# Kernel optimization log

Measured on AMD Instinct MI355X. Metric: run time of the kernel, lower is better.

## Reference

```python
import jax, jax.numpy as jnp
import numpy as np

TAU = 1.0
EPS = 1e-8


def setup_inputs() -> dict:
    key = jax.random.key(0)
    ks = jax.random.split(key, 9)
    B, S, D, R, T = 32, 512, 768, 16, 10
    return {
        "x": jax.random.normal(ks[0], (B, S, D), jnp.float32),
        "A_q": jax.random.normal(ks[1], (T, R, D), jnp.float32),
        "B_q": jax.random.normal(ks[2], (T, D, R), jnp.float32),
        "A_v": jax.random.normal(ks[3], (T, R, D), jnp.float32),
        "B_v": jax.random.normal(ks[4], (T, D, R), jnp.float32),
        "qkv_w": jax.random.normal(ks[5], (3 * D, D), jnp.float32) * 0.02,
        "qkv_b": jax.random.normal(ks[6], (3 * D,), jnp.float32) * 0.02,
        "gate_logits": jax.random.normal(ks[7], (T,), jnp.float32),
        "alpha": jax.random.normal(ks[8], (T,), jnp.float32),
    }


def _delta(x, A, B, coef):
    # A: [T,r,d] (torch Linear weight), B: [T,d,r]
    # per-adapter normalized output: (x @ A_t^T @ B_t^T) / (||A_t||_F * ||B_t||_F + eps)
    norm = (jnp.sqrt(jnp.sum(A * A, axis=(1, 2)))
            * jnp.sqrt(jnp.sum(B * B, axis=(1, 2))) + EPS)  # [T]
    w = coef / norm  # [T], folds beta_t * alpha_t / norm_t into the contraction
    h = jnp.einsum('bsd,trd->bstr', x, A)          # [B,S,T,r] tiny rank intermediate
    return jnp.einsum('bstr,t,tdr->bsd', h, w, B)  # weighted sum over tasks


def reference(x, A_q, B_q, A_v, B_v, qkv_w, qkv_b, gate_logits, alpha):
    # deterministic gate: beta = softmax(logits / tau) (Gumbel noise omitted for a
    # reproducible reference of delta = sum_t beta_t * alpha_t * normalized_adapter_t)
    beta = jax.nn.softmax(gate_logits / TAU)
    coef = beta * alpha
    delta_q = _delta(x, A_q, B_q, coef)
    delta_v = _delta(x, A_v, B_v, coef)
    qkv = jnp.einsum('bsd,ed->bse', x, qkv_w) + qkv_b  # [B,S,3D]
    D = x.shape[-1]
    qkv = qkv.at[..., :D].add(delta_q)
    qkv = qkv.at[..., -D:].add(delta_v)
    return qkv
```

## Files before the change

### kernel.cpp

```cpp
#include <hip/hip_runtime.h>

typedef unsigned short u16;
typedef unsigned int   u32;
typedef __bf16 bf16x8 __attribute__((ext_vector_type(8)));
typedef float  f32x4  __attribute__((ext_vector_type(4)));

#define N_TOT 2304

__device__ __forceinline__ u16 f32_to_bf16(float f) {
  u32 u = __float_as_uint(f);
  u32 r = (u + 0x7FFFu + ((u >> 16) & 1u)) >> 16;
  return (u16)r;
}
__device__ __forceinline__ float bf16_to_f32(u16 h) {
  return __uint_as_float(((u32)h) << 16);
}

__device__ __forceinline__ void gload_lds16(const void* gsrc, void* lds) {
  __builtin_amdgcn_global_load_lds(
      (const __attribute__((address_space(1))) void*)gsrc,
      (__attribute__((address_space(3))) void*)lds, 16, 0, 0);
}

__global__ void norms_kernel(const float* __restrict__ Aq, const float* __restrict__ Bq,
                             const float* __restrict__ Av, const float* __restrict__ Bv,
                             float* __restrict__ sumsq) {
  int b = blockIdx.x;
  int which = b / 10, t = b % 10;
  const float* src =
      (which == 0 ? Aq : which == 1 ? Bq : which == 2 ? Av : Bv) + t * 12288;
  float s = 0.f;
  for (int i = threadIdx.x; i < 12288; i += 256) { float v = src[i]; s += v * v; }
  for (int off = 32; off > 0; off >>= 1) s += __shfl_down(s, off, 64);
  __shared__ float red[4];
  if ((threadIdx.x & 63) == 0) red[threadIdx.x >> 6] = s;
  __syncthreads();
  if (threadIdx.x == 0) sumsq[b] = red[0] + red[1] + red[2] + red[3];
}

__global__ void weights_kernel(const float* __restrict__ logits, const float* __restrict__ alpha,
                               const float* __restrict__ sumsq,
                               float* __restrict__ wq, float* __restrict__ wv) {
  int t = threadIdx.x;
  if (t >= 10) return;
  float m = -1e30f;
  for (int i = 0; i < 10; ++i) m = fmaxf(m, logits[i]);
  float sum = 0.f;
  for (int i = 0; i < 10; ++i) sum += expf(logits[i] - m);
  float coef = (expf(logits[t] - m) / sum) * alpha[t];
  wq[t] = coef / (sqrtf(sumsq[t])      * sqrtf(sumsq[10 + t]) + 1e-8f);
  wv[t] = coef / (sqrtf(sumsq[20 + t]) * sqrtf(sumsq[30 + t]) + 1e-8f);
}

__global__ __launch_bounds__(256) void build_weff(
    const float* __restrict__ qkv_w,
    const float* __restrict__ Aq, const float* __restrict__ Bq,
    const float* __restrict__ Av, const float* __restrict__ Bv,
    const float* __restrict__ wq, const float* __restrict__ wv,
    u16* __restrict__ Whi, u16* __restrict__ Wlo) {
  __shared__ float As[160][64];
  __shared__ float Bs[160][32];
  __shared__ float wsh[16];

  const int k0 = blockIdx.x * 64;
  const int n0 = blockIdx.y * 32;
  const int tid = threadIdx.x;
  const int nl = tid >> 3;
  const int kg = tid & 7;

  float acc[8] = {0, 0, 0, 0, 0, 0, 0, 0};
  const bool is_q = (n0 < 768);
  const bool is_v = (n0 >= 1536);
  if (is_q || is_v) {
    const float* A  = is_q ? Aq : Av;
    const float* Bm = is_q ? Bq : Bv;
    const float* w  = is_q ? wq : wv;
    const int noff = is_q ? n0 : (n0 - 1536);
    for (int i = tid; i < 10240; i += 256)
      As[i >> 6][i & 63] = A[(i >> 6) * 768 + k0 + (i & 63)];
    for (int i = tid; i < 5120; i += 256) {
      int tr = i >> 5, n = i & 31;
      Bs[tr][n] = Bm[(tr >> 4) * 12288 + (noff + n) * 16 + (tr & 15)];
    }
    if (tid < 10) wsh[tid] = w[tid];
    __syncthreads();
    for (int tr = 0; tr < 160; ++tr) {
      float wb = wsh[tr >> 4] * Bs[tr][nl];
#pragma unroll
      for (int j = 0; j < 8; ++j) acc[j] += wb * As[tr][kg * 8 + j];
    }
  }
  const int n = n0 + nl;
  const size_t base = (size_t)n * 768 + k0 + kg * 8;
#pragma unroll
  for (int j = 0; j < 8; ++j) {
    float v = qkv_w[base + j] + acc[j];
    u16 h = f32_to_bf16(v);
    u16 l = f32_to_bf16(v - bf16_to_f32(h));
    Whi[base + j] = h;
    Wlo[base + j] = l;
  }
}

__global__ void split_x(const float* __restrict__ x, u16* __restrict__ Xhi, u16* __restrict__ Xlo) {
  int i4 = blockIdx.x * 256 + threadIdx.x;
  if (i4 >= 3145728) return;
  float4 v = ((const float4*)x)[i4];
  u32 h0 = f32_to_bf16(v.x), h1 = f32_to_bf16(v.y), h2 = f32_to_bf16(v.z), h3 = f32_to_bf16(v.w);
  u32 l0 = f32_to_bf16(v.x - bf16_to_f32((u16)h0));
  u32 l1 = f32_to_bf16(v.y - bf16_to_f32((u16)h1));
  u32 l2 = f32_to_bf16(v.z - bf16_to_f32((u16)h2));
  u32 l3 = f32_to_bf16(v.w - bf16_to_f32((u16)h3));
  ((uint2*)Xhi)[i4] = make_uint2(h0 | (h1 << 16), h2 | (h3 << 16));
  ((uint2*)Xlo)[i4] = make_uint2(l0 | (l1 << 16), l2 | (l3 << 16));
}

__global__ __launch_bounds__(512, 2) void gemm_kc(
    const u16* __restrict__ Xhi, const u16* __restrict__ Xlo,
    const u16* __restrict__ Whi, const u16* __restrict__ Wlo,
    const float* __restrict__ bias, float* __restrict__ out) {
  extern __shared__ char smem[];

  const int tid  = threadIdx.x;
  const int lane = tid & 63;
  const int wid  = tid >> 6;

  const int bid = blockIdx.x;
  const int swz = (bid & 7) * 72 + (bid >> 3);
  const int m0 = (swz / 9) << 8;
  const int n0 = (swz % 9) << 8;

  const int wm = (wid >> 2) << 7;
  const int wn = (wid & 3) << 6;
  const int fl = lane & 15, fs = lane >> 4;

  int aFrag[8], bFrag[4];
#pragma unroll
  for (int i = 0; i < 8; ++i) {
    int R = wm + i * 16 + fl;
    int pr = R >> 1;
    int u = (fs + ((R & 1) << 2)) ^ (pr & 7);
    aFrag[i] = (pr * 8 + u) * 16;
  }
#pragma unroll
  for (int j = 0; j < 4; ++j) {
    int R = wn + j * 16 + fl;
    int pr = R >> 1;
    int u = (fs + ((R & 1) << 2)) ^ (pr & 7);
    bFrag[j] = (pr * 8 + u) * 16;
  }

  int ldsByte[2];
  long aSrcOff[2], bSrcOff[2];
#pragma unroll
  for (int jj = 0; jj < 2; ++jj) {
    int P = jj * 512 + tid;
    int pr = P >> 3, p = P & 7;
    int u = p ^ (pr & 7);
    int r = (pr << 1) | (u >> 2);
    int s = u & 3;
    ldsByte[jj]  = P * 16;
    aSrcOff[jj] = (long)(m0 + r) * 768 + s * 8;
    bSrcOff[jj] = (long)(n0 + r) * 768 + s * 8;
  }

  auto stage = [&](int t2, int bufi) {
    int tc = t2 > 71 ? 71 : t2;
    int reg = tc / 24;
    int ksrc = (tc - reg * 24) << 5;
    const u16* xb = (reg == 2) ? Xlo : Xhi;
    const u16* wb = (reg == 1) ? Wlo : Whi;
    char* base = smem + bufi * 32768;
    gload_lds16(xb + aSrcOff[0] + ksrc, base + ldsByte[0]);
    gload_lds16(xb + aSrcOff[1] + ksrc, base + ldsByte[1]);
    gload_lds16(wb + bSrcOff[0] + ksrc, base + 16384 + ldsByte[0]);
    gload_lds16(wb + bSrcOff[1] + ksrc, base + 16384 + ldsByte[1]);
  };

  f32x4 acc[8][4] = {};

  stage(0, 0);
  stage(1, 1);
  asm volatile("s_waitcnt vmcnt(4)" ::: "memory");
  __builtin_amdgcn_sched_barrier(0);
  __builtin_amdgcn_s_barrier();

  for (int t = 0; t < 72; ++t) {
    char* bufA = smem + (t & 3) * 32768;
    char* bufB = bufA + 16384;
    bf16x8 a[8], b[4];
#pragma unroll
    for (int i = 0; i < 8; ++i) a[i] = *(const bf16x8*)(bufA + aFrag[i]);
#pragma unroll
    for (int j = 0; j < 4; ++j) b[j] = *(const bf16x8*)(bufB + bFrag[j]);

    stage(t + 2, (t + 2) & 3);
    asm volatile("s_waitcnt vmcnt(4)" ::: "memory");
    __builtin_amdgcn_sched_barrier(0);
    __builtin_amdgcn_s_barrier();

    __builtin_amdgcn_s_setprio(1);
#pragma unroll
    for (int i = 0; i < 8; ++i)
#pragma unroll
      for (int j = 0; j < 4; ++j)
        acc[i][j] = __builtin_amdgcn_mfma_f32_16x16x32_bf16(a[i], b[j], acc[i][j], 0, 0, 0);
    __builtin_amdgcn_s_setprio(0);
  }

#pragma unroll
  for (int j = 0; j < 4; ++j) {
    const int n = n0 + wn + j * 16 + fl;
    const float bj = bias[n];
#pragma unroll
    for (int i = 0; i < 8; ++i) {
      const int mbase = m0 + wm + i * 16 + (fs << 2);
#pragma unroll
      for (int r = 0; r < 4; ++r)
        out[(size_t)(mbase + r) * N_TOT + n] = acc[i][j][r] + bj;
    }
  }
}

extern "C" void kernel_launch(void* const* d_in, const int* in_sizes, int n_in,
                              void* d_out, int out_size, void* d_ws, size_t ws_size,
                              hipStream_t stream) {
  const float* x     = (const float*)d_in[0];
  const float* Aq    = (const float*)d_in[1];
  const float* Bq    = (const float*)d_in[2];
  const float* Av    = (const float*)d_in[3];
  const float* Bv    = (const float*)d_in[4];
  const float* qkvw  = (const float*)d_in[5];
  const float* qkvb  = (const float*)d_in[6];
  const float* gate  = (const float*)d_in[7];
  const float* alpha = (const float*)d_in[8];
  float* out = (float*)d_out;

  char* ws = (char*)d_ws;
  float* sumsq = (float*)ws;
  float* wq    = (float*)(ws + 256);
  float* wv    = (float*)(ws + 512);
  u16* Whi = (u16*)(ws + 1024);
  u16* Wlo = Whi + 1769472;
  u16* Xhi = Wlo + 1769472;
  u16* Xlo = Xhi + 12582912;

  static bool attr_set = false;
  if (!attr_set) {
    hipFuncSetAttribute((const void*)gemm_kc,
                        hipFuncAttributeMaxDynamicSharedMemorySize, 131072);
    attr_set = true;
  }

  hipLaunchKernelGGL(norms_kernel,   dim3(40),     dim3(256), 0, stream, Aq, Bq, Av, Bv, sumsq);
  hipLaunchKernelGGL(weights_kernel, dim3(1),      dim3(64),  0, stream, gate, alpha, sumsq, wq, wv);
  hipLaunchKernelGGL(build_weff,     dim3(12, 72), dim3(256), 0, stream, qkvw, Aq, Bq, Av, Bv, wq, wv, Whi, Wlo);
  hipLaunchKernelGGL(split_x,        dim3(12288),  dim3(256), 0, stream, x, Xhi, Xlo);
  hipLaunchKernelGGL(gemm_kc,        dim3(576),    dim3(512), 131072, stream,
                     Xhi, Xlo, Whi, Wlo, qkvb, out);
}
```

Before: 447.4 us.

## Split GEMM main loop into two barrier-fenced phases interleaving LDS reads with MFMA

Splits each K-step of the GEMM main loop into two halves. The first half loads four A fragments and all B fragments, issues the next stage's global-to-LDS loads, then runs 16 MFMAs. The second half loads the remaining four A fragments and runs the other 16 MFMAs. Extra workgroup barriers and explicit lgkmcnt waits enforce a ping-pong style schedule across waves, so LDS reads of one wave can overlap MFMAs of another and peak register pressure drops. The cost is two additional s_barriers per iteration. The attribute-caching flag in the host launcher is also removed, so hipFuncSetAttribute is called on every launch.

```diff
diff --git a/kernel.cpp b/kernel.cpp
--- a/kernel.cpp
+++ b/kernel.cpp
@@ -184,28 +184,77 @@
   asm volatile("s_waitcnt vmcnt(4)" ::: "memory");
   __builtin_amdgcn_sched_barrier(0);
   __builtin_amdgcn_s_barrier();
+  __builtin_amdgcn_sched_barrier(0);
 
   for (int t = 0; t < 72; ++t) {
     char* bufA = smem + (t & 3) * 32768;
     char* bufB = bufA + 16384;
-    bf16x8 a[8], b[4];
-#pragma unroll
-    for (int i = 0; i < 8; ++i) a[i] = *(const bf16x8*)(bufA + aFrag[i]);
-#pragma unroll
-    for (int j = 0; j < 4; ++j) b[j] = *(const bf16x8*)(bufB + bFrag[j]);
-
+
+    bf16x8 a0 = *(const bf16x8*)(bufA + aFrag[0]);
+    bf16x8 a1 = *(const bf16x8*)(bufA + aFrag[1]);
+    bf16x8 a2 = *(const bf16x8*)(bufA + aFrag[2]);
+    bf16x8 a3 = *(const bf16x8*)(bufA + aFrag[3]);
+    bf16x8 b0 = *(const bf16x8*)(bufB + bFrag[0]);
+    bf16x8 b1 = *(const bf16x8*)(bufB + bFrag[1]);
+    bf16x8 b2 = *(const bf16x8*)(bufB + bFrag[2]);
+    bf16x8 b3 = *(const bf16x8*)(bufB + bFrag[3]);
     stage(t + 2, (t + 2) & 3);
+    __builtin_amdgcn_sched_barrier(0);
+    __builtin_amdgcn_s_barrier();
+    asm volatile("s_waitcnt lgkmcnt(0)" ::: "memory");
+    __builtin_amdgcn_sched_barrier(0);
+    __builtin_amdgcn_s_setprio(1);
+    acc[0][0] = __builtin_amdgcn_mfma_f32_16x16x32_bf16(a0, b0, acc[0][0], 0, 0, 0);
+    acc[0][1] = __builtin_amdgcn_mfma_f32_16x16x32_bf16(a0, b1, acc[0][1], 0, 0, 0);
+    acc[0][2] = __builtin_amdgcn_mfma_f32_16x16x32_bf16(a0, b2, acc[0][2], 0, 0, 0);
+    acc[0][3] = __builtin_amdgcn_mfma_f32_16x16x32_bf16(a0, b3, acc[0][3], 0, 0, 0);
+    acc[1][0] = __builtin_amdgcn_mfma_f32_16x16x32_bf16(a1, b0, acc[1][0], 0, 0, 0);
+    acc[1][1] = __builtin_amdgcn_mfma_f32_16x16x32_bf16(a1, b1, acc[1][1], 0, 0, 0);
+    acc[1][2] = __builtin_amdgcn_mfma_f32_16x16x32_bf16(a1, b2, acc[1][2], 0, 0, 0);
+    acc[1][3] = __builtin_amdgcn_mfma_f32_16x16x32_bf16(a1, b3, acc[1][3], 0, 0, 0);
+    acc[2][0] = __builtin_amdgcn_mfma_f32_16x16x32_bf16(a2, b0, acc[2][0], 0, 0, 0);
+    acc[2][1] = __builtin_amdgcn_mfma_f32_16x16x32_bf16(a2, b1, acc[2][1], 0, 0, 0);
+    acc[2][2] = __builtin_amdgcn_mfma_f32_16x16x32_bf16(a2, b2, acc[2][2], 0, 0, 0);
+    acc[2][3] = __builtin_amdgcn_mfma_f32_16x16x32_bf16(a2, b3, acc[2][3], 0, 0, 0);
+    acc[3][0] = __builtin_amdgcn_mfma_f32_16x16x32_bf16(a3, b0, acc[3][0], 0, 0, 0);
+    acc[3][1] = __builtin_amdgcn_mfma_f32_16x16x32_bf16(a3, b1, acc[3][1], 0, 0, 0);
+    acc[3][2] = __builtin_amdgcn_mfma_f32_16x16x32_bf16(a3, b2, acc[3][2], 0, 0, 0);
+    acc[3][3] = __builtin_amdgcn_mfma_f32_16x16x32_bf16(a3, b3, acc[3][3], 0, 0, 0);
+    __builtin_amdgcn_s_setprio(0);
+    __builtin_amdgcn_sched_barrier(0);
+    __builtin_amdgcn_s_barrier();
+    __builtin_amdgcn_sched_barrier(0);
+
+    bf16x8 a4 = *(const bf16x8*)(bufA + aFrag[4]);
+    bf16x8 a5 = *(const bf16x8*)(bufA + aFrag[5]);
+    bf16x8 a6 = *(const bf16x8*)(bufA + aFrag[6]);
+    bf16x8 a7 = *(const bf16x8*)(bufA + aFrag[7]);
     asm volatile("s_waitcnt vmcnt(4)" ::: "memory");
     __builtin_amdgcn_sched_barrier(0);
     __builtin_amdgcn_s_barrier();
-
+    asm volatile("s_waitcnt lgkmcnt(0)" ::: "memory");
+    __builtin_amdgcn_sched_barrier(0);
     __builtin_amdgcn_s_setprio(1);
-#pragma unroll
-    for (int i = 0; i < 8; ++i)
-#pragma unroll
-      for (int j = 0; j < 4; ++j)
-        acc[i][j] = __builtin_amdgcn_mfma_f32_16x16x32_bf16(a[i], b[j], acc[i][j], 0, 0, 0);
+    acc[4][0] = __builtin_amdgcn_mfma_f32_16x16x32_bf16(a4, b0, acc[4][0], 0, 0, 0);
+    acc[4][1] = __builtin_amdgcn_mfma_f32_16x16x32_bf16(a4, b1, acc[4][1], 0, 0, 0);
+    acc[4][2] = __builtin_amdgcn_mfma_f32_16x16x32_bf16(a4, b2, acc[4][2], 0, 0, 0);
+    acc[4][3] = __builtin_amdgcn_mfma_f32_16x16x32_bf16(a4, b3, acc[4][3], 0, 0, 0);
+    acc[5][0] = __builtin_amdgcn_mfma_f32_16x16x32_bf16(a5, b0, acc[5][0], 0, 0, 0);
+    acc[5][1] = __builtin_amdgcn_mfma_f32_16x16x32_bf16(a5, b1, acc[5][1], 0, 0, 0);
+    acc[5][2] = __builtin_amdgcn_mfma_f32_16x16x32_bf16(a5, b2, acc[5][2], 0, 0, 0);
+    acc[5][3] = __builtin_amdgcn_mfma_f32_16x16x32_bf16(a5, b3, acc[5][3], 0, 0, 0);
+    acc[6][0] = __builtin_amdgcn_mfma_f32_16x16x32_bf16(a6, b0, acc[6][0], 0, 0, 0);
+    acc[6][1] = __builtin_amdgcn_mfma_f32_16x16x32_bf16(a6, b1, acc[6][1], 0, 0, 0);
+    acc[6][2] = __builtin_amdgcn_mfma_f32_16x16x32_bf16(a6, b2, acc[6][2], 0, 0, 0);
+    acc[6][3] = __builtin_amdgcn_mfma_f32_16x16x32_bf16(a6, b3, acc[6][3], 0, 0, 0);
+    acc[7][0] = __builtin_amdgcn_mfma_f32_16x16x32_bf16(a7, b0, acc[7][0], 0, 0, 0);
+    acc[7][1] = __builtin_amdgcn_mfma_f32_16x16x32_bf16(a7, b1, acc[7][1], 0, 0, 0);
+    acc[7][2] = __builtin_amdgcn_mfma_f32_16x16x32_bf16(a7, b2, acc[7][2], 0, 0, 0);
+    acc[7][3] = __builtin_amdgcn_mfma_f32_16x16x32_bf16(a7, b3, acc[7][3], 0, 0, 0);
     __builtin_amdgcn_s_setprio(0);
+    __builtin_amdgcn_sched_barrier(0);
+    __builtin_amdgcn_s_barrier();
+    __builtin_amdgcn_sched_barrier(0);
   }
 
 #pragma unroll
@@ -245,12 +294,8 @@
   u16* Xhi = Wlo + 1769472;
   u16* Xlo = Xhi + 12582912;
 
-  static bool attr_set = false;
-  if (!attr_set) {
-    hipFuncSetAttribute((const void*)gemm_kc,
-                        hipFuncAttributeMaxDynamicSharedMemorySize, 131072);
-    attr_set = true;
-  }
+  hipFuncSetAttribute((const void*)gemm_kc,
+                      hipFuncAttributeMaxDynamicSharedMemorySize, 131072);
 
   hipLaunchKernelGGL(norms_kernel,   dim3(40),     dim3(256), 0, stream, Aq, Bq, Av, Bv, sumsq);
   hipLaunchKernelGGL(weights_kernel, dim3(1),      dim3(64),  0, stream, gate, alpha, sumsq, wq, wv);
```

After: 465.4 us. 4.0% more time.

## Drop X low-part split pass and software-pipeline LDS fragment loads in GEMM

Applied to the files above, without the earlier changes.

Removes the Xlo residual (x is now only rounded to bf16), so the split GEMM runs 48 K-steps instead of 72 and split_x writes half as much. The main loop is restructured into ping-pong register buffers: half the A fragments and all B fragments for the next tile are loaded from LDS after the barrier while the second MFMA cluster runs, overlapping LDS reads with MFMA. Offsets shrink to 32-bit ints. Accuracy drops because the x·Whi low-order term is gone, which may exceed tolerance.

```diff
diff --git a/kernel.cpp b/kernel.cpp
--- a/kernel.cpp
+++ b/kernel.cpp
@@ -102,21 +102,16 @@
   }
 }
 
-__global__ void split_x(const float* __restrict__ x, u16* __restrict__ Xhi, u16* __restrict__ Xlo) {
+__global__ void split_x(const float* __restrict__ x, u16* __restrict__ Xhi) {
   int i4 = blockIdx.x * 256 + threadIdx.x;
   if (i4 >= 3145728) return;
   float4 v = ((const float4*)x)[i4];
   u32 h0 = f32_to_bf16(v.x), h1 = f32_to_bf16(v.y), h2 = f32_to_bf16(v.z), h3 = f32_to_bf16(v.w);
-  u32 l0 = f32_to_bf16(v.x - bf16_to_f32((u16)h0));
-  u32 l1 = f32_to_bf16(v.y - bf16_to_f32((u16)h1));
-  u32 l2 = f32_to_bf16(v.z - bf16_to_f32((u16)h2));
-  u32 l3 = f32_to_bf16(v.w - bf16_to_f32((u16)h3));
   ((uint2*)Xhi)[i4] = make_uint2(h0 | (h1 << 16), h2 | (h3 << 16));
-  ((uint2*)Xlo)[i4] = make_uint2(l0 | (l1 << 16), l2 | (l3 << 16));
 }
 
 __global__ __launch_bounds__(512, 2) void gemm_kc(
-    const u16* __restrict__ Xhi, const u16* __restrict__ Xlo,
+    const u16* __restrict__ Xhi,
     const u16* __restrict__ Whi, const u16* __restrict__ Wlo,
     const float* __restrict__ bias, float* __restrict__ out) {
   extern __shared__ char smem[];
@@ -151,7 +146,7 @@
   }
 
   int ldsByte[2];
-  long aSrcOff[2], bSrcOff[2];
+  int aSrcOff[2], bSrcOff[2];
 #pragma unroll
   for (int jj = 0; jj < 2; ++jj) {
     int P = jj * 512 + tid;
@@ -159,53 +154,119 @@
     int u = p ^ (pr & 7);
     int r = (pr << 1) | (u >> 2);
     int s = u & 3;
-    ldsByte[jj]  = P * 16;
-    aSrcOff[jj] = (long)(m0 + r) * 768 + s * 8;
-    bSrcOff[jj] = (long)(n0 + r) * 768 + s * 8;
+    ldsByte[jj] = P * 16;
+    aSrcOff[jj] = (m0 + r) * 768 + s * 8;
+    bSrcOff[jj] = (n0 + r) * 768 + s * 8;
   }
 
   auto stage = [&](int t2, int bufi) {
-    int tc = t2 > 71 ? 71 : t2;
-    int reg = tc / 24;
-    int ksrc = (tc - reg * 24) << 5;
-    const u16* xb = (reg == 2) ? Xlo : Xhi;
-    const u16* wb = (reg == 1) ? Wlo : Whi;
+    int tc = t2 > 47 ? 47 : t2;
+    int kk = tc >= 24 ? tc - 24 : tc;
+    const u16* wb = tc >= 24 ? Wlo : Whi;
+    int ksrc = kk << 5;
     char* base = smem + bufi * 32768;
-    gload_lds16(xb + aSrcOff[0] + ksrc, base + ldsByte[0]);
-    gload_lds16(xb + aSrcOff[1] + ksrc, base + ldsByte[1]);
+    gload_lds16(Xhi + aSrcOff[0] + ksrc, base + ldsByte[0]);
+    gload_lds16(Xhi + aSrcOff[1] + ksrc, base + ldsByte[1]);
     gload_lds16(wb + bSrcOff[0] + ksrc, base + 16384 + ldsByte[0]);
     gload_lds16(wb + bSrcOff[1] + ksrc, base + 16384 + ldsByte[1]);
   };
 
   f32x4 acc[8][4] = {};
+  bf16x8 aX[4], bX[4], aY[4], bY[4], g2[4];
+
+#define CLUSTER1(CA, CB)                                                              \
+  __builtin_amdgcn_s_setprio(1);                                                      \
+  acc[0][0] = __builtin_amdgcn_mfma_f32_16x16x32_bf16(CA[0], CB[0], acc[0][0], 0, 0, 0); \
+  acc[0][1] = __builtin_amdgcn_mfma_f32_16x16x32_bf16(CA[0], CB[1], acc[0][1], 0, 0, 0); \
+  acc[0][2] = __builtin_amdgcn_mfma_f32_16x16x32_bf16(CA[0], CB[2], acc[0][2], 0, 0, 0); \
+  acc[0][3] = __builtin_amdgcn_mfma_f32_16x16x32_bf16(CA[0], CB[3], acc[0][3], 0, 0, 0); \
+  acc[1][0] = __builtin_amdgcn_mfma_f32_16x16x32_bf16(CA[1], CB[0], acc[1][0], 0, 0, 0); \
+  acc[1][1] = __builtin_amdgcn_mfma_f32_16x16x32_bf16(CA[1], CB[1], acc[1][1], 0, 0, 0); \
+  acc[1][2] = __builtin_amdgcn_mfma_f32_16x16x32_bf16(CA[1], CB[2], acc[1][2], 0, 0, 0); \
+  acc[1][3] = __builtin_amdgcn_mfma_f32_16x16x32_bf16(CA[1], CB[3], acc[1][3], 0, 0, 0); \
+  acc[2][0] = __builtin_amdgcn_mfma_f32_16x16x32_bf16(CA[2], CB[0], acc[2][0], 0, 0, 0); \
+  acc[2][1] = __builtin_amdgcn_mfma_f32_16x16x32_bf16(CA[2], CB[1], acc[2][1], 0, 0, 0); \
+  acc[2][2] = __builtin_amdgcn_mfma_f32_16x16x32_bf16(CA[2], CB[2], acc[2][2], 0, 0, 0); \
+  acc[2][3] = __builtin_amdgcn_mfma_f32_16x16x32_bf16(CA[2], CB[3], acc[2][3], 0, 0, 0); \
+  acc[3][0] = __builtin_amdgcn_mfma_f32_16x16x32_bf16(CA[3], CB[0], acc[3][0], 0, 0, 0); \
+  acc[3][1] = __builtin_amdgcn_mfma_f32_16x16x32_bf16(CA[3], CB[1], acc[3][1], 0, 0, 0); \
+  acc[3][2] = __builtin_amdgcn_mfma_f32_16x16x32_bf16(CA[3], CB[2], acc[3][2], 0, 0, 0); \
+  acc[3][3] = __builtin_amdgcn_mfma_f32_16x16x32_bf16(CA[3], CB[3], acc[3][3], 0, 0, 0); \
+  __builtin_amdgcn_s_setprio(0);
+
+#define CLUSTER2(CB)                                                                  \
+  __builtin_amdgcn_s_setprio(1);                                                      \
+  acc[4][0] = __builtin_amdgcn_mfma_f32_16x16x32_bf16(g2[0], CB[0], acc[4][0], 0, 0, 0); \
+  acc[4][1] = __builtin_amdgcn_mfma_f32_16x16x32_bf16(g2[0], CB[1], acc[4][1], 0, 0, 0); \
+  acc[4][2] = __builtin_amdgcn_mfma_f32_16x16x32_bf16(g2[0], CB[2], acc[4][2], 0, 0, 0); \
+  acc[4][3] = __builtin_amdgcn_mfma_f32_16x16x32_bf16(g2[0], CB[3], acc[4][3], 0, 0, 0); \
+  acc[5][0] = __builtin_amdgcn_mfma_f32_16x16x32_bf16(g2[1], CB[0], acc[5][0], 0, 0, 0); \
+  acc[5][1] = __builtin_amdgcn_mfma_f32_16x16x32_bf16(g2[1], CB[1], acc[5][1], 0, 0, 0); \
+  acc[5][2] = __builtin_amdgcn_mfma_f32_16x16x32_bf16(g2[1], CB[2], acc[5][2], 0, 0, 0); \
+  acc[5][3] = __builtin_amdgcn_mfma_f32_16x16x32_bf16(g2[1], CB[3], acc[5][3], 0, 0, 0); \
+  acc[6][0] = __builtin_amdgcn_mfma_f32_16x16x32_bf16(g2[2], CB[0], acc[6][0], 0, 0, 0); \
+  acc[6][1] = __builtin_amdgcn_mfma_f32_16x16x32_bf16(g2[2], CB[1], acc[6][1], 0, 0, 0); \
+  acc[6][2] = __builtin_amdgcn_mfma_f32_16x16x32_bf16(g2[2], CB[2], acc[6][2], 0, 0, 0); \
+  acc[6][3] = __builtin_amdgcn_mfma_f32_16x16x32_bf16(g2[2], CB[3], acc[6][3], 0, 0, 0); \
+  acc[7][0] = __builtin_amdgcn_mfma_f32_16x16x32_bf16(g2[3], CB[0], acc[7][0], 0, 0, 0); \
+  acc[7][1] = __builtin_amdgcn_mfma_f32_16x16x32_bf16(g2[3], CB[1], acc[7][1], 0, 0, 0); \
+  acc[7][2] = __builtin_amdgcn_mfma_f32_16x16x32_bf16(g2[3], CB[2], acc[7][2], 0, 0, 0); \
+  acc[7][3] = __builtin_amdgcn_mfma_f32_16x16x32_bf16(g2[3], CB[3], acc[7][3], 0, 0, 0); \
+  __builtin_amdgcn_s_setprio(0);
+
+#define TILE_BODY(T, CA, CB, NA, NB)                                           \
+  {                                                                            \
+    const int tcur = (T);                                                      \
+    char* bufA = smem + (tcur & 3) * 32768;                                    \
+    g2[0] = *(const bf16x8*)(bufA + aFrag[4]);                                 \
+    g2[1] = *(const bf16x8*)(bufA + aFrag[5]);                                 \
+    g2[2] = *(const bf16x8*)(bufA + aFrag[6]);                                 \
+    g2[3] = *(const bf16x8*)(bufA + aFrag[7]);                                 \
+    stage(tcur + 2, (tcur + 2) & 3);                                           \
+    __builtin_amdgcn_sched_barrier(0);                                         \
+    CLUSTER1(CA, CB)                                                           \
+    __builtin_amdgcn_sched_barrier(0);                                         \
+    asm volatile("s_waitcnt vmcnt(4)" ::: "memory");                           \
+    __builtin_amdgcn_sched_barrier(0);                                         \
+    __builtin_amdgcn_s_barrier();                                              \
+    __builtin_amdgcn_sched_barrier(0);                                         \
+    char* nA = smem + ((tcur + 1) & 3) * 32768;                                \
+    char* nB = nA + 16384;                                                     \
+    NB[0] = *(const bf16x8*)(nB + bFrag[0]);                                   \
+    NB[1] = *(const bf16x8*)(nB + bFrag[1]);                                   \
+    NB[2] = *(const bf16x8*)(nB + bFrag[2]);                                   \
+    NB[3] = *(const bf16x8*)(nB + bFrag[3]);                                   \
+    NA[0] = *(const bf16x8*)(nA + aFrag[0]);                                   \
+    NA[1] = *(const bf16x8*)(nA + aFrag[1]);                                   \
+    NA[2] = *(const bf16x8*)(nA + aFrag[2]);                                   \
+    NA[3] = *(const bf16x8*)(nA + aFrag[3]);                                   \
+    __builtin_amdgcn_sched_barrier(0);                                         \
+    CLUSTER2(CB)                                                               \
+    __builtin_amdgcn_sched_barrier(0);                                         \
+  }
 
   stage(0, 0);
   stage(1, 1);
   asm volatile("s_waitcnt vmcnt(4)" ::: "memory");
   __builtin_amdgcn_sched_barrier(0);
   __builtin_amdgcn_s_barrier();
-
-  for (int t = 0; t < 72; ++t) {
-    char* bufA = smem + (t & 3) * 32768;
-    char* bufB = bufA + 16384;
-    bf16x8 a[8], b[4];
-#pragma unroll
-    for (int i = 0; i < 8; ++i) a[i] = *(const bf16x8*)(bufA + aFrag[i]);
-#pragma unroll
-    for (int j = 0; j < 4; ++j) b[j] = *(const bf16x8*)(bufB + bFrag[j]);
-
-    stage(t + 2, (t + 2) & 3);
-    asm volatile("s_waitcnt vmcnt(4)" ::: "memory");
-    __builtin_amdgcn_sched_barrier(0);
-    __builtin_amdgcn_s_barrier();
-
-    __builtin_amdgcn_s_setprio(1);
-#pragma unroll
-    for (int i = 0; i < 8; ++i)
-#pragma unroll
-      for (int j = 0; j < 4; ++j)
-        acc[i][j] = __builtin_amdgcn_mfma_f32_16x16x32_bf16(a[i], b[j], acc[i][j], 0, 0, 0);
-    __builtin_amdgcn_s_setprio(0);
+  __builtin_amdgcn_sched_barrier(0);
+  {
+    char* bA = smem;
+    char* bB = smem + 16384;
+    bX[0] = *(const bf16x8*)(bB + bFrag[0]);
+    bX[1] = *(const bf16x8*)(bB + bFrag[1]);
+    bX[2] = *(const bf16x8*)(bB + bFrag[2]);
+    bX[3] = *(const bf16x8*)(bB + bFrag[3]);
+    aX[0] = *(const bf16x8*)(bA + aFrag[0]);
+    aX[1] = *(const bf16x8*)(bA + aFrag[1]);
+    aX[2] = *(const bf16x8*)(bA + aFrag[2]);
+    aX[3] = *(const bf16x8*)(bA + aFrag[3]);
+  }
+
+  for (int tt = 0; tt < 48; tt += 2) {
+    TILE_BODY(tt,     aX, bX, aY, bY)
+    TILE_BODY(tt + 1, aY, bY, aX, bX)
   }
 
 #pragma unroll
@@ -220,6 +281,9 @@
         out[(size_t)(mbase + r) * N_TOT + n] = acc[i][j][r] + bj;
     }
   }
+#undef TILE_BODY
+#undef CLUSTER1
+#undef CLUSTER2
 }
 
 extern "C" void kernel_launch(void* const* d_in, const int* in_sizes, int n_in,
@@ -243,19 +307,14 @@
   u16* Whi = (u16*)(ws + 1024);
   u16* Wlo = Whi + 1769472;
   u16* Xhi = Wlo + 1769472;
-  u16* Xlo = Xhi + 12582912;
-
-  static bool attr_set = false;
-  if (!attr_set) {
-    hipFuncSetAttribute((const void*)gemm_kc,
-                        hipFuncAttributeMaxDynamicSharedMemorySize, 131072);
-    attr_set = true;
-  }
+
+  hipFuncSetAttribute((const void*)gemm_kc,
+                      hipFuncAttributeMaxDynamicSharedMemorySize, 131072);
 
   hipLaunchKernelGGL(norms_kernel,   dim3(40),     dim3(256), 0, stream, Aq, Bq, Av, Bv, sumsq);
   hipLaunchKernelGGL(weights_kernel, dim3(1),      dim3(64),  0, stream, gate, alpha, sumsq, wq, wv);
   hipLaunchKernelGGL(build_weff,     dim3(12, 72), dim3(256), 0, stream, qkvw, Aq, Bq, Av, Bv, wq, wv, Whi, Wlo);
-  hipLaunchKernelGGL(split_x,        dim3(12288),  dim3(256), 0, stream, x, Xhi, Xlo);
+  hipLaunchKernelGGL(split_x,        dim3(12288),  dim3(256), 0, stream, x, Xhi);
   hipLaunchKernelGGL(gemm_kc,        dim3(576),    dim3(512), 131072, stream,
-                     Xhi, Xlo, Whi, Wlo, qkvb, out);
-}
+                     Xhi, Whi, Wlo, qkvb, out);
+}
```

New measurement: 380.9 us. -14.9%, faster.
